# Performance work log

Hardware: AMD Instinct MI355X
Metric: run time of the kernel (lower is better)

Reference implementation:

```python
import jax, jax.numpy as jnp
import numpy as np

B, S, D = 4, 2048, 1024
H, DK = 16, 64
NEG = -1e9


def setup_inputs() -> dict:
    key = jax.random.key(0)
    ks = jax.random.split(key, 6)
    hidden_states = jax.random.normal(ks[0], (B, S, D), dtype=jnp.float32)
    # evidence-constrained mask: causal mask plus random evidence restriction
    causal = jnp.tril(jnp.ones((S, S), dtype=bool))
    evid = jax.random.bernoulli(ks[1], 0.7, (S, S))
    allowed = causal & (evid | jnp.eye(S, dtype=bool))  # diag always allowed
    attention_mask = jnp.where(allowed, 0.0, NEG).astype(jnp.float32)
    scale = 0.02
    Wq = jax.random.normal(ks[2], (H * DK, D), dtype=jnp.float32) * scale
    Wk = jax.random.normal(ks[3], (H * DK, D), dtype=jnp.float32) * scale
    Wv = jax.random.normal(ks[4], (H * DK, D), dtype=jnp.float32) * scale
    Wo = jax.random.normal(ks[5], (D, H * DK), dtype=jnp.float32) * scale
    return {"hidden_states": hidden_states, "attention_mask": attention_mask,
            "Wq": Wq, "Wk": Wk, "Wv": Wv, "Wo": Wo}


def reference(hidden_states, attention_mask, Wq, Wk, Wv, Wo):
    b, s, _ = hidden_states.shape
    # nn.Linear(bias=False): y = x @ W.T ; reshape to (B,H,S,DK)
    def proj(x, W):
        y = jnp.einsum('bsd,ed->bse', x, W)
        return y.reshape(b, s, H, DK).transpose(0, 2, 1, 3)
    q = proj(hidden_states, Wq)
    k = proj(hidden_states, Wk)
    v = proj(hidden_states, Wv)
    logits = jnp.einsum('bhqd,bhkd->bhqk', q, k) / jnp.sqrt(jnp.float32(DK))
    logits = logits + attention_mask[None, None, :, :]
    attn = jax.nn.softmax(logits, axis=-1)
    ctx = jnp.einsum('bhqk,bhkd->bhqd', attn, v)
    ctx = ctx.transpose(0, 2, 1, 3).reshape(b, s, H * DK)
    out = jnp.einsum('bse,de->bsd', ctx, Wo)
    return out
```

## Files before the change

### kernel.cpp

```cpp
#include <hip/hip_runtime.h>
#include <hip/hip_bf16.h>
#include <math.h>

#define B_  4
#define S_  2048
#define D_  1024
#define H_  16
#define DK_ 64
#define M_  (B_*S_)
#define E_  (H_*DK_)
#define LOG2E  1.4426950408889634f
#define QSCALE 0.18033688011112042f

typedef short  bf16x8 __attribute__((ext_vector_type(8)));
typedef float  f32x4  __attribute__((ext_vector_type(4)));
typedef unsigned short u16;
typedef unsigned int   u32;
typedef unsigned long long u64;

__device__ __forceinline__ u16 f2b(float x) {
    __hip_bfloat16 h = __float2bfloat16(x);
    return *(u16*)&h;
}

__device__ __forceinline__ void async16(const u16* g, u16* l) {
    __builtin_amdgcn_global_load_lds(
        (const __attribute__((address_space(1))) unsigned int*)g,
        (__attribute__((address_space(3))) unsigned int*)l, 16, 0, 0);
}

#define XN8 (M_ * D_ / 8)
#define WN8 (E_ * D_ / 8)
__global__ __launch_bounds__(256)
void cvt_all(const float* __restrict__ X,
             const float* __restrict__ Wq, const float* __restrict__ Wk,
             const float* __restrict__ Wv, const float* __restrict__ Wo,
             u16* __restrict__ Xb,
             u16* __restrict__ Wqb, u16* __restrict__ Wkb,
             u16* __restrict__ Wvb, u16* __restrict__ Wob) {
    int idx = blockIdx.x * 256 + threadIdx.x;
    const float* s; u16* d; int off;
    if (idx < XN8) { s = X; d = Xb; off = idx; }
    else {
        int j = idx - XN8;
        int which = j / WN8; off = j - which * WN8;
        s = which == 0 ? Wq : which == 1 ? Wk : which == 2 ? Wv : Wo;
        d = which == 0 ? Wqb : which == 1 ? Wkb : which == 2 ? Wvb : Wob;
    }
    const float4* s4 = (const float4*)s;
    float4 a = s4[2 * off], b = s4[2 * off + 1];
    u16 o[8] = {f2b(a.x), f2b(a.y), f2b(a.z), f2b(a.w),
                f2b(b.x), f2b(b.y), f2b(b.z), f2b(b.w)};
    *(uint4*)(d + (size_t)8 * off) = *(const uint4*)o;
}

__global__ __launch_bounds__(256)
void maskcvt(const float* __restrict__ mask, u32* __restrict__ bits) {
    const int w   = threadIdx.x >> 6;
    const int lane = threadIdx.x & 63;
    const int row = blockIdx.x * 4 + w;
    const float* mr = mask + (size_t)row * S_;
    u64* br = (u64*)(bits + (size_t)row * (S_ / 32));
    #pragma unroll
    for (int i = 0; i < S_ / 64; i++) {
        float v = mr[i * 64 + lane];
        u64 bal = __ballot(v == 0.0f);
        if (lane == 0) br[i] = bal;
    }
}

__device__ __forceinline__ void gemm_core(
    const u16* __restrict__ Ag, const u16* __restrict__ Bg, int K,
    int bm, int bn, u16* As, u16* Bs, f32x4 (&acc)[4][4])
{
    const int tid  = threadIdx.x;
    const int w    = tid >> 6, lane = tid & 63;
    const int l15  = lane & 15, quad = lane >> 4;
    const int wm   = (w >> 1) * 64, wn = (w & 1) * 64;
    const int srow = lane >> 3;
    const int sg   = (lane & 7) ^ srow;
    const int sx   = l15 & 7;

    for (int k0 = 0; k0 < K; k0 += 64) {
        __syncthreads();
        #pragma unroll
        for (int i = 0; i < 4; i++) {
            const int row = w * 32 + i * 8 + srow;
            async16(Ag + (size_t)(bm + row) * K + k0 + sg * 8,
                    As + (size_t)(w * 32 + i * 8) * 64);
            async16(Bg + (size_t)(bn + row) * K + k0 + sg * 8,
                    Bs + (size_t)(w * 32 + i * 8) * 64);
        }
        __syncthreads();

        #pragma unroll
        for (int s = 0; s < 2; s++) {
            bf16x8 af[4], bf[4];
            #pragma unroll
            for (int i = 0; i < 4; i++)
                af[i] = *(const bf16x8*)(As + (size_t)(wm + i * 16 + l15) * 64
                                            + (((s * 4 + quad) ^ sx) * 8));
            #pragma unroll
            for (int j = 0; j < 4; j++)
                bf[j] = *(const bf16x8*)(Bs + (size_t)(wn + j * 16 + l15) * 64
                                            + (((s * 4 + quad) ^ sx) * 8));
            #pragma unroll
            for (int i = 0; i < 4; i++)
                #pragma unroll
                for (int j = 0; j < 4; j++)
                    acc[i][j] = __builtin_amdgcn_mfma_f32_16x16x32_bf16(af[i], bf[j], acc[i][j], 0, 0, 0);
        }
    }
}

__global__ __launch_bounds__(256)
void gemm_qkv(const u16* __restrict__ Xb,
              const u16* __restrict__ Wqb, const u16* __restrict__ Wkb,
              const u16* __restrict__ Wvb,
              u16* __restrict__ Qm, u16* __restrict__ Km, u16* __restrict__ Vt)
{
    __shared__ u16 As[128 * 64];
    __shared__ u16 Bs[128 * 64];
    const int bm    = blockIdx.x * 128;
    const int nb    = blockIdx.y;
    const int which = nb >> 3;
    const int col0  = (nb & 7) * 128;
    const u16* Bg = which == 0 ? Wqb : which == 1 ? Wkb : Wvb;

    f32x4 acc[4][4] = {};
    gemm_core(Xb, Bg, D_, bm, col0, As, Bs, acc);

    const int tid = threadIdx.x;
    const int w   = tid >> 6, lane = tid & 63;
    const int l15 = lane & 15, quad = lane >> 4;
    const int wm  = (w >> 1) * 64, wn = (w & 1) * 64;

    if (which == 2) {
        #pragma unroll
        for (int i = 0; i < 4; i++)
            #pragma unroll
            for (int j = 0; j < 4; j++) {
                int c    = col0 + wn + j * 16 + l15;
                int tok0 = bm + wm + i * 16 + quad * 4;
                u16 pk[4] = {f2b(acc[i][j][0]), f2b(acc[i][j][1]),
                             f2b(acc[i][j][2]), f2b(acc[i][j][3])};
                size_t idx = (((size_t)((tok0 >> 11) * E_ + c)) << 11) + (tok0 & 2047);
                *(uint2*)(Vt + idx) = *(const uint2*)pk;
            }
    } else {
        u16* Cm = which == 0 ? Qm : Km;
        const float sc = which == 0 ? QSCALE : 1.0f;
        #pragma unroll
        for (int i = 0; i < 4; i++)
            #pragma unroll
            for (int j = 0; j < 4; j++)
                #pragma unroll
                for (int r = 0; r < 4; r++) {
                    int row = bm + wm + i * 16 + quad * 4 + r;
                    int c   = col0 + wn + j * 16 + l15;
                    Cm[(size_t)row * E_ + c] = f2b(acc[i][j][r] * sc);
                }
    }
}

__global__ __launch_bounds__(256)
void gemm_out(const u16* __restrict__ Cmx, const u16* __restrict__ Wob,
              float* __restrict__ out)
{
    __shared__ u16 As[128 * 64];
    __shared__ u16 Bs[128 * 64];
    const int bm = blockIdx.x * 128;
    const int bn = blockIdx.y * 128;

    f32x4 acc[4][4] = {};
    gemm_core(Cmx, Wob, E_, bm, bn, As, Bs, acc);

    const int tid = threadIdx.x;
    const int w   = tid >> 6, lane = tid & 63;
    const int l15 = lane & 15, quad = lane >> 4;
    const int wm  = (w >> 1) * 64, wn = (w & 1) * 64;
    #pragma unroll
    for (int i = 0; i < 4; i++)
        #pragma unroll
        for (int j = 0; j < 4; j++)
            #pragma unroll
            for (int r = 0; r < 4; r++)
                out[(size_t)(bm + wm + i * 16 + quad * 4 + r) * D_ + bn + wn + j * 16 + l15]
                    = acc[i][j][r];
}

__global__ __launch_bounds__(512)
void flash_attn(const u16* __restrict__ Q, const u16* __restrict__ Kc,
                const u16* __restrict__ Vt, const u32* __restrict__ bits,
                u16* __restrict__ ctx)
{
    const int bh  = blockIdx.x;
    const int qt  = (gridDim.y - 1) - blockIdx.y;
    const int b   = bh >> 4, h = bh & 15;
    const int tid = threadIdx.x;
    const int w   = tid >> 6, lane = tid & 63;
    const int l15 = lane & 15, quad = lane >> 4;
    const int q0  = qt * 128;
    const int nkt = 2 * qt + 2;

    __shared__ u16 Ks[64 * 64];
    __shared__ u16 Vs[64 * 64];
    __shared__ u16 Ps[8][16 * 64];

    const u16* qb = Q + ((size_t)(b * S_ + q0 + w * 16 + l15)) * E_ + h * DK_;
    bf16x8 qf0 = *(const bf16x8*)(qb + quad * 8);
    bf16x8 qf1 = *(const bf16x8*)(qb + 32 + quad * 8);

    f32x4 acc[4] = {};
    float lsum = 0.f;

    const int sr = lane >> 3;
    const int sg = (lane & 7) ^ sr;
    const int sx = l15 & 7;
    u16* Pw = &Ps[w][0];
    const u32* mrow = bits + (size_t)(q0 + w * 16 + l15) * (S_ / 32);

    for (int kt = 0; kt < nkt; ++kt) {
        const int k0 = kt * 64;

        u64 mword = *(const u64*)(mrow + (k0 >> 5));

        __syncthreads();
        {
            const int row8 = w * 8;
            async16(Kc + ((size_t)(b * S_ + k0 + row8 + sr)) * E_ + h * DK_ + sg * 8,
                    Ks + row8 * 64);
            async16(Vt + ((size_t)(bh * DK_ + row8 + sr)) * S_ + k0 + sg * 8,
                    Vs + row8 * 64);
        }
        __syncthreads();

        f32x4 st[4] = {};
        #pragma unroll
        for (int t = 0; t < 4; t++) {
            bf16x8 kf0 = *(const bf16x8*)(Ks + (t * 16 + l15) * 64 + ((quad ^ sx) * 8));
            bf16x8 kf1 = *(const bf16x8*)(Ks + (t * 16 + l15) * 64 + (((4 + quad) ^ sx) * 8));
            st[t] = __builtin_amdgcn_mfma_f32_16x16x32_bf16(kf0, qf0, st[t], 0, 0, 0);
            st[t] = __builtin_amdgcn_mfma_f32_16x16x32_bf16(kf1, qf1, st[t], 0, 0, 0);
        }

        #pragma unroll
        for (int t = 0; t < 4; t++) {
            u32 nib = (u32)(mword >> (t * 16 + quad * 4)) & 0xF;
            float p0 = (nib & 1) ? exp2f(st[t][0]) : 0.0f;
            float p1 = (nib & 2) ? exp2f(st[t][1]) : 0.0f;
            float p2 = (nib & 4) ? exp2f(st[t][2]) : 0.0f;
            float p3 = (nib & 8) ? exp2f(st[t][3]) : 0.0f;
            lsum += (p0 + p1) + (p2 + p3);
            u16 pk[4] = {f2b(p0), f2b(p1), f2b(p2), f2b(p3)};
            *(uint2*)(Pw + l15 * 64 + (((2 * t + (quad >> 1)) ^ sx) * 8) + (quad & 1) * 4)
                = *(const uint2*)pk;
        }

        #pragma unroll
        for (int sb = 0; sb < 2; sb++) {
            bf16x8 pf = *(const bf16x8*)(Pw + l15 * 64 + (((4 * sb + quad) ^ sx) * 8));
            #pragma unroll
            for (int nt = 0; nt < 4; nt++) {
                bf16x8 vf = *(const bf16x8*)(Vs + (nt * 16 + l15) * 64 + (((4 * sb + quad) ^ sx) * 8));
                acc[nt] = __builtin_amdgcn_mfma_f32_16x16x32_bf16(pf, vf, acc[nt], 0, 0, 0);
            }
        }
    }

    lsum += __shfl_xor(lsum, 16, 64);
    lsum += __shfl_xor(lsum, 32, 64);
    float linv = 1.0f / lsum;
    float ir[4];
    #pragma unroll
    for (int r = 0; r < 4; r++) ir[r] = __shfl(linv, quad * 4 + r, 16);
    #pragma unroll
    for (int r = 0; r < 4; r++) {
        size_t orow = ((size_t)(b * S_ + q0 + w * 16 + quad * 4 + r)) * E_ + h * DK_;
        #pragma unroll
        for (int nt = 0; nt < 4; nt++)
            ctx[orow + nt * 16 + l15] = f2b(acc[nt][r] * ir[r]);
    }
}

extern "C" void kernel_launch(void* const* d_in, const int* in_sizes, int n_in,
                              void* d_out, int out_size, void* d_ws, size_t ws_size,
                              hipStream_t stream) {
    const float* X    = (const float*)d_in[0];
    const float* mask = (const float*)d_in[1];
    const float* Wq   = (const float*)d_in[2];
    const float* Wk   = (const float*)d_in[3];
    const float* Wv   = (const float*)d_in[4];
    const float* Wo   = (const float*)d_in[5];
    float* out = (float*)d_out;

    char* p = (char*)d_ws;
    u16* Qm  = (u16*)p; p += (size_t)M_ * E_ * 2;
    u16* Km  = (u16*)p; p += (size_t)M_ * E_ * 2;
    u16* Vt  = (u16*)p; p += (size_t)M_ * E_ * 2;
    u16* Wqb = (u16*)p; p += (size_t)E_ * D_ * 2;
    u16* Wkb = (u16*)p; p += (size_t)E_ * D_ * 2;
    u16* Wvb = (u16*)p; p += (size_t)E_ * D_ * 2;
    u16* Wob = (u16*)p; p += (size_t)D_ * E_ * 2;
    u32* Mb  = (u32*)p; p += (size_t)S_ * (S_ / 32) * 4;
    u16* Xb  = (u16*)p;
    u16* Cm  = Xb;

    cvt_all<<<(XN8 + 4 * WN8 + 255) / 256, 256, 0, stream>>>(
        X, Wq, Wk, Wv, Wo, Xb, Wqb, Wkb, Wvb, Wob);
    maskcvt<<<S_ / 4, 256, 0, stream>>>(mask, Mb);

    gemm_qkv<<<dim3(M_ / 128, 24), 256, 0, stream>>>(Xb, Wqb, Wkb, Wvb, Qm, Km, Vt);

    flash_attn<<<dim3(B_ * H_, S_ / 128), 512, 0, stream>>>(Qm, Km, Vt, Mb, Cm);

    gemm_out<<<dim3(M_ / 128, D_ / 128), 256, 0, stream>>>(Cm, Wob, out);
}
```

Measured before the change: 282.7 us.

## Double-buffer K/V tiles and keep P in registers for PV MFMA

Double-buffers the K and V shared-memory tiles so the async global-to-LDS loads for the next key tile are issued before computing the current tile, which removes one barrier per iteration. It also drops the per-wave P staging buffer: probabilities are packed to bf16 in registers with v_cvt_pk_bf16_f32, and V fragments are gathered with a matching permutation of the reduction index so P no longer round-trips through LDS. In exchange LDS use for K/V doubles, and the single barrier now relies on vmcnt waits for the async loads to be correct.

Measured after the change: 278.4 us. About the same (-1.5%).

```diff
diff --git a/kernel.cpp b/kernel.cpp
--- a/kernel.cpp
+++ b/kernel.cpp
@@ -21,6 +21,12 @@
 __device__ __forceinline__ u16 f2b(float x) {
     __hip_bfloat16 h = __float2bfloat16(x);
     return *(u16*)&h;
+}
+
+__device__ __forceinline__ u32 cvtpk(float lo, float hi) {
+    u32 r;
+    asm("v_cvt_pk_bf16_f32 %0, %1, %2" : "=v"(r) : "v"(lo), "v"(hi));
+    return r;
 }
 
 __device__ __forceinline__ void async16(const u16* g, u16* l) {
@@ -203,9 +209,8 @@
     const int q0  = qt * 128;
     const int nkt = 2 * qt + 2;
 
-    __shared__ u16 Ks[64 * 64];
-    __shared__ u16 Vs[64 * 64];
-    __shared__ u16 Ps[8][16 * 64];
+    __shared__ u16 Ks[2][64 * 64];
+    __shared__ u16 Vs[2][64 * 64];
 
     const u16* qb = Q + ((size_t)(b * S_ + q0 + w * 16 + l15)) * E_ + h * DK_;
     bf16x8 qf0 = *(const bf16x8*)(qb + quad * 8);
@@ -217,55 +222,76 @@
     const int sr = lane >> 3;
     const int sg = (lane & 7) ^ sr;
     const int sx = l15 & 7;
-    u16* Pw = &Ps[w][0];
+    const int qh = quad >> 1, ql = quad & 1;
+
+    const int voff00 = (((0 + qh) ^ sx) * 8 + ql * 4) * 2;
+    const int voff01 = (((2 + qh) ^ sx) * 8 + ql * 4) * 2;
+    const int voff10 = (((4 + qh) ^ sx) * 8 + ql * 4) * 2;
+    const int voff11 = (((6 + qh) ^ sx) * 8 + ql * 4) * 2;
+
     const u32* mrow = bits + (size_t)(q0 + w * 16 + l15) * (S_ / 32);
-
+    const u16* kg = Kc + ((size_t)(b * S_ + w * 8 + sr)) * E_ + h * DK_ + sg * 8;
+    const u16* vg = Vt + ((size_t)(bh * DK_ + w * 8 + sr)) * S_ + sg * 8;
+
+    async16(kg, &Ks[0][w * 512]); kg += (size_t)64 * E_;
+    async16(vg, &Vs[0][w * 512]); vg += 64;
+    u64 mw_next = *(const u64*)mrow;
+
+    int cur = 0;
     for (int kt = 0; kt < nkt; ++kt) {
-        const int k0 = kt * 64;
-
-        u64 mword = *(const u64*)(mrow + (k0 >> 5));
-
+        const int nxt = cur ^ 1;
         __syncthreads();
-        {
-            const int row8 = w * 8;
-            async16(Kc + ((size_t)(b * S_ + k0 + row8 + sr)) * E_ + h * DK_ + sg * 8,
-                    Ks + row8 * 64);
-            async16(Vt + ((size_t)(bh * DK_ + row8 + sr)) * S_ + k0 + sg * 8,
-                    Vs + row8 * 64);
-        }
-        __syncthreads();
-
+        u64 mw = mw_next;
+        if (kt + 1 < nkt) {
+            async16(kg, &Ks[nxt][w * 512]); kg += (size_t)64 * E_;
+            async16(vg, &Vs[nxt][w * 512]); vg += 64;
+            mw_next = *(const u64*)(mrow + ((kt + 1) << 1));
+        }
+
+        const u16* Kb = Ks[cur];
         f32x4 st[4] = {};
         #pragma unroll
         for (int t = 0; t < 4; t++) {
-            bf16x8 kf0 = *(const bf16x8*)(Ks + (t * 16 + l15) * 64 + ((quad ^ sx) * 8));
-            bf16x8 kf1 = *(const bf16x8*)(Ks + (t * 16 + l15) * 64 + (((4 + quad) ^ sx) * 8));
+            bf16x8 kf0 = *(const bf16x8*)(Kb + (t * 16 + l15) * 64 + ((quad ^ sx) * 8));
+            bf16x8 kf1 = *(const bf16x8*)(Kb + (t * 16 + l15) * 64 + (((4 + quad) ^ sx) * 8));
             st[t] = __builtin_amdgcn_mfma_f32_16x16x32_bf16(kf0, qf0, st[t], 0, 0, 0);
             st[t] = __builtin_amdgcn_mfma_f32_16x16x32_bf16(kf1, qf1, st[t], 0, 0, 0);
         }
 
+        const u64 m2 = mw >> (quad * 4);
+        const u32 mlo = (u32)m2, mhi = (u32)(m2 >> 32);
+        const u32 nib[4] = { mlo & 0xF, (mlo >> 16) & 0xF,
+                             mhi & 0xF, (mhi >> 16) & 0xF };
         #pragma unroll
         for (int t = 0; t < 4; t++) {
-            u32 nib = (u32)(mword >> (t * 16 + quad * 4)) & 0xF;
-            float p0 = (nib & 1) ? exp2f(st[t][0]) : 0.0f;
-            float p1 = (nib & 2) ? exp2f(st[t][1]) : 0.0f;
-            float p2 = (nib & 4) ? exp2f(st[t][2]) : 0.0f;
-            float p3 = (nib & 8) ? exp2f(st[t][3]) : 0.0f;
-            lsum += (p0 + p1) + (p2 + p3);
-            u16 pk[4] = {f2b(p0), f2b(p1), f2b(p2), f2b(p3)};
-            *(uint2*)(Pw + l15 * 64 + (((2 * t + (quad >> 1)) ^ sx) * 8) + (quad & 1) * 4)
-                = *(const uint2*)pk;
-        }
-
+            st[t][0] = (nib[t] & 1) ? exp2f(st[t][0]) : 0.0f;
+            st[t][1] = (nib[t] & 2) ? exp2f(st[t][1]) : 0.0f;
+            st[t][2] = (nib[t] & 4) ? exp2f(st[t][2]) : 0.0f;
+            st[t][3] = (nib[t] & 8) ? exp2f(st[t][3]) : 0.0f;
+            lsum += (st[t][0] + st[t][1]) + (st[t][2] + st[t][3]);
+        }
+
+        const char* Vrow = (const char*)(Vs[cur] + l15 * 64);
         #pragma unroll
         for (int sb = 0; sb < 2; sb++) {
-            bf16x8 pf = *(const bf16x8*)(Pw + l15 * 64 + (((4 * sb + quad) ^ sx) * 8));
+            union { u32 w4[4]; bf16x8 v; } pu;
+            pu.w4[0] = cvtpk(st[2 * sb][0],     st[2 * sb][1]);
+            pu.w4[1] = cvtpk(st[2 * sb][2],     st[2 * sb][3]);
+            pu.w4[2] = cvtpk(st[2 * sb + 1][0], st[2 * sb + 1][1]);
+            pu.w4[3] = cvtpk(st[2 * sb + 1][2], st[2 * sb + 1][3]);
+            const int vA = sb ? voff10 : voff00;
+            const int vB = sb ? voff11 : voff01;
             #pragma unroll
             for (int nt = 0; nt < 4; nt++) {
-                bf16x8 vf = *(const bf16x8*)(Vs + (nt * 16 + l15) * 64 + (((4 * sb + quad) ^ sx) * 8));
-                acc[nt] = __builtin_amdgcn_mfma_f32_16x16x32_bf16(pf, vf, acc[nt], 0, 0, 0);
+                uint2 va = *(const uint2*)(Vrow + nt * 2048 + vA);
+                uint2 vb = *(const uint2*)(Vrow + nt * 2048 + vB);
+                union { u32 w4[4]; bf16x8 v; } vu;
+                vu.w4[0] = va.x; vu.w4[1] = va.y;
+                vu.w4[2] = vb.x; vu.w4[3] = vb.y;
+                acc[nt] = __builtin_amdgcn_mfma_f32_16x16x32_bf16(pu.v, vu.v, acc[nt], 0, 0, 0);
             }
         }
+        cur = nxt;
     }
 
     lsum += __shfl_xor(lsum, 16, 64);
```
